# Performance work log

Measured on AMD Instinct MI355X. Metric: run time of the kernel, lower is better.

## Reference

```python
import jax, jax.numpy as jnp
import numpy as np

H = 1024
S = 2048
B = 16

def setup_inputs() -> dict:
    key = jax.random.key(0)
    k1, k2, k3, k4, k5, k6 = jax.random.split(key, 6)
    hidden = jax.random.normal(k1, (1, B, H), dtype=jnp.float32)
    encoder_outputs = jax.random.normal(k2, (S, B, H), dtype=jnp.float32)
    seq_mask = jax.random.randint(k3, (B, S), 0, 2, dtype=jnp.int32)
    # nn.Linear(2H, H): weight [H, 2H], bias [H]
    lim1 = 1.0 / np.sqrt(2 * H)
    attn_w = jax.random.uniform(k4, (H, 2 * H), minval=-lim1, maxval=lim1, dtype=jnp.float32)
    attn_b = jax.random.uniform(k5, (H,), minval=-lim1, maxval=lim1, dtype=jnp.float32)
    # nn.Linear(H, 1, bias=False): weight [1, H]
    lim2 = 1.0 / np.sqrt(H)
    score_w = jax.random.uniform(k6, (1, H), minval=-lim2, maxval=lim2, dtype=jnp.float32)
    return {"hidden": hidden, "encoder_outputs": encoder_outputs, "seq_mask": seq_mask,
            "attn_w": attn_w, "attn_b": attn_b, "score_w": score_w}

def reference(hidden, encoder_outputs, seq_mask, attn_w, attn_b, score_w):
    # Faithful to: cat([hidden.repeat(S,1,1), encoder_outputs], -1) @ attn_w.T + attn_b
    # Split the concat-linear into two GEMMs (identical math, avoids the big concat).
    h = hidden.shape[-1]
    Wh = attn_w[:, :h]   # acts on repeated hidden
    We = attn_w[:, h:]   # acts on encoder outputs
    # hidden: [1,B,H] broadcasts over S; encoder_outputs: [S,B,H]
    pre = jnp.einsum('obh,kh->obk', hidden, Wh) + jnp.einsum('sbh,kh->sbk', encoder_outputs, We) + attn_b
    proj = jnp.tanh(pre)                               # [S,B,H]
    energies = jnp.einsum('sbh,oh->sbo', proj, score_w)[..., 0]  # [S,B]
    energies = energies.T                              # [B,S] (transpose(0,1) in original)
    energies = jnp.where(seq_mask.astype(bool), jnp.float32(-1e12), energies)
    attn = jax.nn.softmax(energies, axis=1)            # [B,S]
    return attn[:, None, :]                            # [B,1,S]
```

## Files before the change

kernel.cpp:

```cpp
#include <hip/hip_runtime.h>
#include <hip/hip_bf16.h>

#define HDIM 1024
#define SEQ 2048
#define BATCH 16
#define M_TOT (SEQ*BATCH)
#define NBLK 4
#define BM 256
#define BN 256
#define BKT 64
#define NT (HDIM/BKT)

#define NB_ENC ((M_TOT*HDIM)/(8*256))
#define NB_WE  ((HDIM*HDIM)/(8*256))
#define NB_QK  (HDIM)

typedef __attribute__((ext_vector_type(8))) short short8;
typedef __attribute__((ext_vector_type(4))) float f32x4;

typedef const void __attribute__((address_space(1))) gvoid_t;
typedef void __attribute__((address_space(3))) svoid_t;
#define GLD16(gp, lp) __builtin_amdgcn_global_load_lds((gvoid_t*)(gp), (svoid_t*)(lp), 16, 0, 0)
#define VMC(N) asm volatile("s_waitcnt vmcnt(" #N ")" ::: "memory")

static __device__ __forceinline__ unsigned short f2bf(float f) {
    unsigned int x = __float_as_uint(f);
    unsigned int r = (x + 0x7FFFu + ((x >> 16) & 1u)) >> 16;
    return (unsigned short)r;
}

__global__ __launch_bounds__(256) void prep_all(const float* __restrict__ hidden,
                                                const float* __restrict__ enc,
                                                const float* __restrict__ attn_w,
                                                const float* __restrict__ attn_b,
                                                float* __restrict__ q,
                                                __hip_bfloat16* __restrict__ web,
                                                __hip_bfloat16* __restrict__ encb) {
    int bid = blockIdx.x;
    if (bid < NB_ENC) {
        size_t i0 = ((size_t)bid * 256 + threadIdx.x) * 8;
        const float4* s = reinterpret_cast<const float4*>(enc + i0);
        float4 a = s[0], b = s[1];
        union { unsigned short u[8]; short8 v; } cv;
        cv.u[0] = f2bf(a.x); cv.u[1] = f2bf(a.y); cv.u[2] = f2bf(a.z); cv.u[3] = f2bf(a.w);
        cv.u[4] = f2bf(b.x); cv.u[5] = f2bf(b.y); cv.u[6] = f2bf(b.z); cv.u[7] = f2bf(b.w);
        *reinterpret_cast<short8*>((unsigned short*)encb + i0) = cv.v;
        return;
    }
    if (bid < NB_ENC + NB_WE) {
        size_t i0 = ((size_t)(bid - NB_ENC) * 256 + threadIdx.x) * 8;
        int n = (int)(i0 >> 10);
        int h = (int)(i0 & 1023);
        const float4* src = reinterpret_cast<const float4*>(attn_w + (size_t)n * (2 * HDIM) + HDIM + h);
        float4 a = src[0], b = src[1];
        union { unsigned short u[8]; short8 v; } cv;
        cv.u[0] = f2bf(a.x); cv.u[1] = f2bf(a.y); cv.u[2] = f2bf(a.z); cv.u[3] = f2bf(a.w);
        cv.u[4] = f2bf(b.x); cv.u[5] = f2bf(b.y); cv.u[6] = f2bf(b.z); cv.u[7] = f2bf(b.w);
        *reinterpret_cast<short8*>((unsigned short*)web + i0) = cv.v;
        return;
    }
    int k = bid - (NB_ENC + NB_WE);
    int tid = threadIdx.x;
    const float* w = attn_w + (size_t)k * (2 * HDIM);
    float p[BATCH];
#pragma unroll
    for (int b = 0; b < BATCH; b++) p[b] = 0.f;
    for (int h = tid; h < HDIM; h += 256) {
        float wv = w[h];
#pragma unroll
        for (int b = 0; b < BATCH; b++) p[b] += hidden[b * HDIM + h] * wv;
    }
#pragma unroll
    for (int b = 0; b < BATCH; b++) {
        for (int off = 32; off; off >>= 1) p[b] += __shfl_down(p[b], off);
    }
    __shared__ float red[4][BATCH];
    int lane = tid & 63, wid = tid >> 6;
    if (lane == 0) {
#pragma unroll
        for (int b = 0; b < BATCH; b++) red[wid][b] = p[b];
    }
    __syncthreads();
    if (tid < BATCH) {
        float s = red[0][tid] + red[1][tid] + red[2][tid] + red[3][tid] + attn_b[k];
        q[(size_t)tid * HDIM + k] = s;
    }
}

__global__ __launch_bounds__(512, 2) void gemm8(const __hip_bfloat16* __restrict__ encb,
                                                const __hip_bfloat16* __restrict__ web,
                                                const float* __restrict__ qv,
                                                const float* __restrict__ score_w,
                                                float* __restrict__ part) {
    __shared__ __align__(16) char pool[163840];

    int tid = threadIdx.x;
    int lane = tid & 63;
    int wid = tid >> 6;
    int wr = wid >> 2;
    int wc = wid & 3;

    int bid = blockIdx.x;
    int lin = (bid & 7) * 64 + (bid >> 3);
    int bm = lin >> 2;
    int bn = lin & 3;
    int m0 = bm * BM, n0 = bn * BN;

    int srow = tid >> 3;
    int scolb = (((tid & 7) ^ ((tid >> 3) & 7)) << 4);
    const char* eb = (const char*)encb;
    const char* wb = (const char*)web;

    auto STG = [&](const char* g, int ldsoff) {
        GLD16(g + (size_t)srow * 2048 + scolb, pool + ldsoff + wid * 1024);
        GLD16(g + (size_t)(srow + 64) * 2048 + scolb, pool + ldsoff + 8192 + wid * 1024);
    };
    auto APTR = [&](int kt, int h) { return eb + ((size_t)(m0 + h * 128) * HDIM + kt * BKT) * 2; };
    auto BPTR = [&](int kt, int h) { return wb + ((size_t)(n0 + h * 128) * HDIM + kt * BKT) * 2; };
#define ALDS(par, h) ((par) * 32768 + (h) * 16384)
#define BLDS(buf, h) (65536 + (buf) * 32768 + (h) * 16384)

    int lq = lane & 15, lh = lane >> 4;
    int flip = (lane & 7) << 4;
    int pks0 = lq * 128 + ((lh * 16) ^ flip);
    int pks1 = lq * 128 + (((64 + lh * 16)) ^ flip);
    int aFB = wr * 16384;
    int bOFF = (wc >> 1) * 16384 + (wc & 1) * 8192;

    f32x4 acc[8][4];
#pragma unroll
    for (int i = 0; i < 8; i++)
#pragma unroll
        for (int j = 0; j < 4; j++) acc[i][j] = (f32x4)0.f;
    short8 br[4][2];

#define RD8(off) (*reinterpret_cast<const short8*>(pool + (off)))

#define CLUSTER(Q, PAR, BB, STAGE_STMT)                                                   \
    {                                                                                     \
        if ((Q) == 0) {                                                                   \
            _Pragma("unroll") for (int nj = 0; nj < 4; ++nj) {                            \
                br[nj][0] = RD8(65536 + (BB) * 32768 + bOFF + nj * 2048 + pks0);          \
                br[nj][1] = RD8(65536 + (BB) * 32768 + bOFF + nj * 2048 + pks1);          \
            }                                                                             \
        }                                                                                 \
        short8 a0k0 = RD8(aFB + (PAR) * 32768 + (2 * (Q)) * 2048 + pks0);                 \
        short8 a0k1 = RD8(aFB + (PAR) * 32768 + (2 * (Q)) * 2048 + pks1);                 \
        short8 a1k0 = RD8(aFB + (PAR) * 32768 + (2 * (Q) + 1) * 2048 + pks0);             \
        short8 a1k1 = RD8(aFB + (PAR) * 32768 + (2 * (Q) + 1) * 2048 + pks1);             \
        STAGE_STMT;                                                                       \
        __builtin_amdgcn_s_setprio(1);                                                    \
        _Pragma("unroll") for (int nj = 0; nj < 4; ++nj) {                                \
            acc[2 * (Q)][nj] = __builtin_amdgcn_mfma_f32_16x16x32_bf16(a0k0, br[nj][0], acc[2 * (Q)][nj], 0, 0, 0); \
            acc[2 * (Q)][nj] = __builtin_amdgcn_mfma_f32_16x16x32_bf16(a0k1, br[nj][1], acc[2 * (Q)][nj], 0, 0, 0); \
            acc[2 * (Q) + 1][nj] = __builtin_amdgcn_mfma_f32_16x16x32_bf16(a1k0, br[nj][0], acc[2 * (Q) + 1][nj], 0, 0, 0); \
            acc[2 * (Q) + 1][nj] = __builtin_amdgcn_mfma_f32_16x16x32_bf16(a1k1, br[nj][1], acc[2 * (Q) + 1][nj], 0, 0, 0); \
        }                                                                                 \
        __builtin_amdgcn_s_setprio(0);                                                    \
    }

#define TILE(PAR, BB, S1, S2, S3, S4, CLOSE)                                              \
    {                                                                                     \
        CLUSTER(0, PAR, BB, S1);                                                          \
        CLUSTER(1, PAR, BB, S2);                                                          \
        CLUSTER(2, PAR, BB, S3);                                                          \
        CLUSTER(3, PAR, BB, S4);                                                          \
        CLOSE;                                                                            \
        __builtin_amdgcn_s_barrier();                                                     \
        __builtin_amdgcn_sched_barrier(0);                                                \
    }

    STG(APTR(0, 0), ALDS(0, 0));
    STG(APTR(0, 1), ALDS(0, 1));
    STG(BPTR(0, 0), BLDS(0, 0));
    STG(BPTR(0, 1), BLDS(0, 1));
    STG(BPTR(1, 0), BLDS(1, 0));
    STG(BPTR(1, 1), BLDS(1, 1));
    VMC(4);
    __builtin_amdgcn_s_barrier();
    __builtin_amdgcn_sched_barrier(0);

#pragma unroll 1
    for (int J = 0; J < 2; ++J) {
        int t = 6 * J;
        TILE(0, 0, STG(APTR(t + 1, 0), ALDS(1, 0)), STG(APTR(t + 1, 1), ALDS(1, 1)),
                   STG(BPTR(t + 2, 0), BLDS(2, 0)), STG(BPTR(t + 2, 1), BLDS(2, 1)), VMC(4));
        TILE(1, 1, STG(APTR(t + 2, 0), ALDS(0, 0)), STG(APTR(t + 2, 1), ALDS(0, 1)),
                   STG(BPTR(t + 3, 0), BLDS(0, 0)), STG(BPTR(t + 3, 1), BLDS(0, 1)), VMC(4));
        TILE(0, 2, STG(APTR(t + 3, 0), ALDS(1, 0)), STG(APTR(t + 3, 1), ALDS(1, 1)),
                   STG(BPTR(t + 4, 0), BLDS(1, 0)), STG(BPTR(t + 4, 1), BLDS(1, 1)), VMC(4));
        TILE(1, 0, STG(APTR(t + 4, 0), ALDS(0, 0)), STG(APTR(t + 4, 1), ALDS(0, 1)),
                   STG(BPTR(t + 5, 0), BLDS(2, 0)), STG(BPTR(t + 5, 1), BLDS(2, 1)), VMC(4));
        TILE(0, 1, STG(APTR(t + 5, 0), ALDS(1, 0)), STG(APTR(t + 5, 1), ALDS(1, 1)),
                   STG(BPTR(t + 6, 0), BLDS(0, 0)), STG(BPTR(t + 6, 1), BLDS(0, 1)), VMC(4));
        TILE(1, 2, STG(APTR(t + 6, 0), ALDS(0, 0)), STG(APTR(t + 6, 1), ALDS(0, 1)),
                   STG(BPTR(t + 7, 0), BLDS(1, 0)), STG(BPTR(t + 7, 1), BLDS(1, 1)), VMC(4));
    }
    TILE(0, 0, STG(APTR(13, 0), ALDS(1, 0)), STG(APTR(13, 1), ALDS(1, 1)),
               STG(BPTR(14, 0), BLDS(2, 0)), STG(BPTR(14, 1), BLDS(2, 1)), VMC(4));
    TILE(1, 1, STG(APTR(14, 0), ALDS(0, 0)), STG(APTR(14, 1), ALDS(0, 1)),
               STG(BPTR(15, 0), BLDS(0, 0)), STG(BPTR(15, 1), BLDS(0, 1)), VMC(4));
    TILE(0, 2, STG(APTR(15, 0), ALDS(1, 0)), STG(APTR(15, 1), ALDS(1, 1)), , , VMC(0));
    TILE(1, 0, , , , , );

    float* q_lds = reinterpret_cast<float*>(pool);
    float* sc_lds = reinterpret_cast<float*>(pool + 16384);
    float* red = reinterpret_cast<float*>(pool + 17408);
    {
        int qb = tid >> 5;
        int kl = (tid & 31) * 8;
        const float4* src = reinterpret_cast<const float4*>(qv + (size_t)qb * HDIM + n0 + kl);
        float4 v0 = src[0], v1 = src[1];
        *reinterpret_cast<float4*>(&q_lds[qb * 256 + kl]) = v0;
        *reinterpret_cast<float4*>(&q_lds[qb * 256 + kl + 4]) = v1;
        if (tid < BN) sc_lds[tid] = score_w[n0 + tid];
    }
    __syncthreads();

#pragma unroll
    for (int mi = 0; mi < 8; ++mi) {
#pragma unroll
        for (int r = 0; r < 4; ++r) {
            int b = lh * 4 + r;
            float s = 0.f;
#pragma unroll
            for (int nj = 0; nj < 4; ++nj) {
                int kl = wc * 64 + nj * 16 + lq;
                float v = acc[mi][nj][r] + q_lds[b * 256 + kl];
                float t = 1.f - 2.f / (__expf(2.f * v) + 1.f);
                s += sc_lds[kl] * t;
            }
            int row = wr * 128 + mi * 16 + b;
            red[(wc * 256 + row) * 20 + lq] = s;
        }
    }
    __syncthreads();
    if (tid < BM) {
        float t = 0.f;
#pragma unroll
        for (int w4 = 0; w4 < 4; ++w4) {
            const f32x4* p = reinterpret_cast<const f32x4*>(&red[(w4 * 256 + tid) * 20]);
#pragma unroll
            for (int i = 0; i < 4; ++i) {
                f32x4 v = p[i];
                t += v[0] + v[1] + v[2] + v[3];
            }
        }
        part[(size_t)bn * M_TOT + m0 + tid] = t;
    }
#undef CLUSTER
#undef TILE
#undef RD8
#undef ALDS
#undef BLDS
}

__global__ __launch_bounds__(256) void softmax_kernel(const float* __restrict__ part,
                                                      const int* __restrict__ mask,
                                                      float* __restrict__ out) {
    int b = blockIdx.x;
    int tid = threadIdx.x;
    __shared__ float e_lds[SEQ];
    __shared__ float red[4], red2[4];
    int lane = tid & 63, wid = tid >> 6;
    float lmax = -3.4e38f;
    for (int it = 0; it < SEQ / 256; ++it) {
        int s = it * 256 + tid;
        size_t m = (size_t)s * BATCH + b;
        float e = 0.f;
#pragma unroll
        for (int c = 0; c < NBLK; c++) e += part[(size_t)c * M_TOT + m];
        if (mask[(size_t)b * SEQ + s]) e = -1e12f;
        e_lds[s] = e;
        lmax = fmaxf(lmax, e);
    }
    for (int off = 32; off; off >>= 1) lmax = fmaxf(lmax, __shfl_xor(lmax, off));
    if (lane == 0) red[wid] = lmax;
    __syncthreads();
    float gmax = fmaxf(fmaxf(red[0], red[1]), fmaxf(red[2], red[3]));
    float lsum = 0.f;
    for (int it = 0; it < SEQ / 256; ++it) {
        int s = it * 256 + tid;
        float p = __expf(e_lds[s] - gmax);
        e_lds[s] = p;
        lsum += p;
    }
    for (int off = 32; off; off >>= 1) lsum += __shfl_xor(lsum, off);
    if (lane == 0) red2[wid] = lsum;
    __syncthreads();
    float inv = 1.f / (red2[0] + red2[1] + red2[2] + red2[3]);
    for (int it = 0; it < SEQ / 256; ++it) {
        int s = it * 256 + tid;
        out[(size_t)b * SEQ + s] = e_lds[s] * inv;
    }
}

extern "C" void kernel_launch(void* const* d_in, const int* in_sizes, int n_in,
                              void* d_out, int out_size, void* d_ws, size_t ws_size,
                              hipStream_t stream) {
    const float* hidden   = (const float*)d_in[0];
    const float* enc      = (const float*)d_in[1];
    const int*   seq_mask = (const int*)d_in[2];
    const float* attn_w   = (const float*)d_in[3];
    const float* attn_b   = (const float*)d_in[4];
    const float* score_w  = (const float*)d_in[5];
    float* out = (float*)d_out;

    char* ws = (char*)d_ws;
    float* q = (float*)ws;
    __hip_bfloat16* web = (__hip_bfloat16*)(ws + 65536);
    float* part = (float*)(ws + 65536 + 2 * 1024 * 1024);
    __hip_bfloat16* encb = (__hip_bfloat16*)(ws + 65536 + 3 * 1024 * 1024);

    prep_all<<<dim3(NB_ENC + NB_WE + NB_QK), dim3(256), 0, stream>>>(hidden, enc, attn_w, attn_b, q, web, encb);
    gemm8<<<dim3(NBLK * (M_TOT / BM)), dim3(512), 0, stream>>>(encb, web, q, score_w, part);
    softmax_kernel<<<dim3(BATCH), dim3(256), 0, stream>>>(part, seq_mask, out);
}
```

Baseline: 116.4 us.

## Compact unmasked rows and skip GEMM work for masked sequence positions

After: 127.2 us. +9.2%, slower.

```diff
diff --git a/kernel.cpp b/kernel.cpp
--- a/kernel.cpp
+++ b/kernel.cpp
@@ -29,22 +29,77 @@
     return (unsigned short)r;
 }
 
+__global__ __launch_bounds__(1024) void scan_kernel(const int* __restrict__ mask,
+                                                    int* __restrict__ rowidx,
+                                                    int* __restrict__ jof,
+                                                    int* __restrict__ nkeep) {
+    int t = threadIdx.x;
+    int flags[32];
+    int cnt = 0;
+#pragma unroll
+    for (int i = 0; i < 32; ++i) {
+        int m = t * 32 + i;
+        int b = m & 15, s = m >> 4;
+        int f = (mask[(size_t)b * SEQ + s] == 0) ? 1 : 0;
+        flags[i] = f;
+        cnt += f;
+    }
+    int lane = t & 63, wv = t >> 6;
+    int inc = cnt;
+    for (int off = 1; off < 64; off <<= 1) {
+        int o = __shfl_up(inc, off);
+        if (lane >= off) inc += o;
+    }
+    __shared__ int wsum[16], wbase[16];
+    if (lane == 63) wsum[wv] = inc;
+    __syncthreads();
+    if (t == 0) {
+        int acc = 0;
+        for (int w = 0; w < 16; ++w) { wbase[w] = acc; acc += wsum[w]; }
+        nkeep[0] = acc;
+    }
+    __syncthreads();
+    int e = wbase[wv] + inc - cnt;
+#pragma unroll
+    for (int i = 0; i < 32; ++i) {
+        int m = t * 32 + i;
+        if (flags[i]) {
+            rowidx[e] = m;
+            jof[m] = e;
+            e++;
+        }
+    }
+}
+
 __global__ __launch_bounds__(256) void prep_all(const float* __restrict__ hidden,
                                                 const float* __restrict__ enc,
                                                 const float* __restrict__ attn_w,
                                                 const float* __restrict__ attn_b,
+                                                const int* __restrict__ rowidx,
+                                                const int* __restrict__ nkp,
                                                 float* __restrict__ q,
                                                 __hip_bfloat16* __restrict__ web,
                                                 __hip_bfloat16* __restrict__ encb) {
     int bid = blockIdx.x;
     if (bid < NB_ENC) {
-        size_t i0 = ((size_t)bid * 256 + threadIdx.x) * 8;
-        const float4* s = reinterpret_cast<const float4*>(enc + i0);
-        float4 a = s[0], b = s[1];
+        int nkeep = nkp[0];
+        int npad = (nkeep + 255) & ~255;
+        int j = bid * 2 + (threadIdx.x >> 7);
+        if (j >= npad) return;
+        int col = (threadIdx.x & 127) * 8;
+        unsigned short* dst = (unsigned short*)encb + (size_t)j * HDIM + col;
+        if (j >= nkeep) {
+            short8 z = (short8)0;
+            *reinterpret_cast<short8*>(dst) = z;
+            return;
+        }
+        int m = rowidx[j];
+        const float4* s4 = reinterpret_cast<const float4*>(enc + (size_t)m * HDIM + col);
+        float4 a = s4[0], b = s4[1];
         union { unsigned short u[8]; short8 v; } cv;
         cv.u[0] = f2bf(a.x); cv.u[1] = f2bf(a.y); cv.u[2] = f2bf(a.z); cv.u[3] = f2bf(a.w);
         cv.u[4] = f2bf(b.x); cv.u[5] = f2bf(b.y); cv.u[6] = f2bf(b.z); cv.u[7] = f2bf(b.w);
-        *reinterpret_cast<short8*>((unsigned short*)encb + i0) = cv.v;
+        *reinterpret_cast<short8*>(dst) = cv.v;
         return;
     }
     if (bid < NB_ENC + NB_WE) {
@@ -91,6 +146,8 @@
                                                 const __hip_bfloat16* __restrict__ web,
                                                 const float* __restrict__ qv,
                                                 const float* __restrict__ score_w,
+                                                const int* __restrict__ rowidx,
+                                                const int* __restrict__ nkp,
                                                 float* __restrict__ part) {
     __shared__ __align__(16) char pool[163840];
 
@@ -105,6 +162,10 @@
     int bm = lin >> 2;
     int bn = lin & 3;
     int m0 = bm * BM, n0 = bn * BN;
+
+    int nkeep = nkp[0];
+    int npad = (nkeep + 255) & ~255;
+    if (m0 >= npad) return;
 
     int srow = tid >> 3;
     int scolb = (((tid & 7) ^ ((tid >> 3) & 7)) << 4);
@@ -205,7 +266,8 @@
 
     float* q_lds = reinterpret_cast<float*>(pool);
     float* sc_lds = reinterpret_cast<float*>(pool + 16384);
-    float* red = reinterpret_cast<float*>(pool + 17408);
+    int* rowb = reinterpret_cast<int*>(pool + 17408);
+    float* red = reinterpret_cast<float*>(pool + 18432);
     {
         int qb = tid >> 5;
         int kl = (tid & 31) * 8;
@@ -214,6 +276,7 @@
         *reinterpret_cast<float4*>(&q_lds[qb * 256 + kl]) = v0;
         *reinterpret_cast<float4*>(&q_lds[qb * 256 + kl + 4]) = v1;
         if (tid < BN) sc_lds[tid] = score_w[n0 + tid];
+        if (tid < BM) rowb[tid] = (m0 + tid < nkeep) ? (rowidx[m0 + tid] & 15) : 0;
     }
     __syncthreads();
 
@@ -221,16 +284,16 @@
     for (int mi = 0; mi < 8; ++mi) {
 #pragma unroll
         for (int r = 0; r < 4; ++r) {
-            int b = lh * 4 + r;
+            int row = wr * 128 + mi * 16 + lh * 4 + r;
+            int bq = rowb[row];
             float s = 0.f;
 #pragma unroll
             for (int nj = 0; nj < 4; ++nj) {
                 int kl = wc * 64 + nj * 16 + lq;
-                float v = acc[mi][nj][r] + q_lds[b * 256 + kl];
+                float v = acc[mi][nj][r] + q_lds[bq * 256 + kl];
                 float t = 1.f - 2.f / (__expf(2.f * v) + 1.f);
                 s += sc_lds[kl] * t;
             }
-            int row = wr * 128 + mi * 16 + b;
             red[(wc * 256 + row) * 20 + lq] = s;
         }
     }
@@ -257,6 +320,7 @@
 
 __global__ __launch_bounds__(256) void softmax_kernel(const float* __restrict__ part,
                                                       const int* __restrict__ mask,
+                                                      const int* __restrict__ jof,
                                                       float* __restrict__ out) {
     int b = blockIdx.x;
     int tid = threadIdx.x;
@@ -266,11 +330,15 @@
     float lmax = -3.4e38f;
     for (int it = 0; it < SEQ / 256; ++it) {
         int s = it * 256 + tid;
-        size_t m = (size_t)s * BATCH + b;
-        float e = 0.f;
-#pragma unroll
-        for (int c = 0; c < NBLK; c++) e += part[(size_t)c * M_TOT + m];
-        if (mask[(size_t)b * SEQ + s]) e = -1e12f;
+        float e = -1e12f;
+        if (!mask[(size_t)b * SEQ + s]) {
+            int m = s * BATCH + b;
+            int j = jof[m];
+            float acc = 0.f;
+#pragma unroll
+            for (int c = 0; c < NBLK; c++) acc += part[(size_t)c * M_TOT + j];
+            e = acc;
+        }
         e_lds[s] = e;
         lmax = fmaxf(lmax, e);
     }
@@ -310,9 +378,15 @@
     float* q = (float*)ws;
     __hip_bfloat16* web = (__hip_bfloat16*)(ws + 65536);
     float* part = (float*)(ws + 65536 + 2 * 1024 * 1024);
+    int* rowidx = (int*)(ws + 65536 + 2 * 1024 * 1024 + 512 * 1024);
+    int* jof    = (int*)(ws + 65536 + 2 * 1024 * 1024 + 640 * 1024);
+    int* nkeep  = (int*)(ws + 65536 + 2 * 1024 * 1024 + 768 * 1024);
     __hip_bfloat16* encb = (__hip_bfloat16*)(ws + 65536 + 3 * 1024 * 1024);
 
-    prep_all<<<dim3(NB_ENC + NB_WE + NB_QK), dim3(256), 0, stream>>>(hidden, enc, attn_w, attn_b, q, web, encb);
-    gemm8<<<dim3(NBLK * (M_TOT / BM)), dim3(512), 0, stream>>>(encb, web, q, score_w, part);
-    softmax_kernel<<<dim3(BATCH), dim3(256), 0, stream>>>(part, seq_mask, out);
-}
+    scan_kernel<<<dim3(1), dim3(1024), 0, stream>>>(seq_mask, rowidx, jof, nkeep);
+    prep_all<<<dim3(NB_ENC + NB_WE + NB_QK), dim3(256), 0, stream>>>(hidden, enc, attn_w, attn_b,
+                                                                     rowidx, nkeep, q, web, encb);
+    gemm8<<<dim3(NBLK * (M_TOT / BM)), dim3(512), 0, stream>>>(encb, web, q, score_w,
+                                                               rowidx, nkeep, part);
+    softmax_kernel<<<dim3(BATCH), dim3(256), 0, stream>>>(part, seq_mask, jof, out);
+}
```
